# Performance work log

Measured on AMD Instinct MI355X. Metric: run time of the kernel, lower is better.

Reference implementation:

```python
import jax, jax.numpy as jnp
import numpy as np

D_MODEL, NHEAD, D_K = 512, 8, 64
MIN_RBF, MAX_RBF = 0.1, 0.9
MIN_SPREAD, MAX_SPREAD, BASE = 1.0, 6.0, 20.0
LN_EPS = 1e-5


def _layernorm(x, w, b):
    mu = jnp.mean(x, axis=-1, keepdims=True)
    var = jnp.var(x, axis=-1, keepdims=True)
    return (x - mu) * jax.lax.rsqrt(var + LN_EPS) * w + b


def setup_inputs() -> dict:
    key = jax.random.key(0)
    ks = jax.random.split(key, 10)
    B, N = 1, 2048
    inp = {
        "q": jax.random.normal(ks[0], (B, N, D_MODEL), jnp.float32),
        "k": jax.random.normal(ks[1], (B, N, D_MODEL), jnp.float32),
        "v": jax.random.normal(ks[2], (B, N, D_MODEL), jnp.float32),
        "coords": jax.random.normal(ks[3], (B, N, 3), jnp.float32) * 3.0,
        "key_padding_mask": jnp.zeros((B, N), bool),
        # learned params (torch.randn init for projections, LN defaults)
        "q_proj": jax.random.normal(ks[4], (NHEAD, D_MODEL, D_K), jnp.float32),
        "k_proj": jax.random.normal(ks[5], (NHEAD, D_MODEL, D_K), jnp.float32),
        "v_proj": jax.random.normal(ks[6], (NHEAD, D_MODEL, D_K), jnp.float32),
        "q_ln_w": jnp.ones((D_K,), jnp.float32), "q_ln_b": jnp.zeros((D_K,), jnp.float32),
        "k_ln_w": jnp.ones((D_K,), jnp.float32), "k_ln_b": jnp.zeros((D_K,), jnp.float32),
        "v_ln_w": jnp.ones((D_K,), jnp.float32), "v_ln_b": jnp.zeros((D_K,), jnp.float32),
        "out_w": jax.random.normal(ks[7], (D_MODEL, D_MODEL), jnp.float32) / np.sqrt(D_MODEL),
        "out_b": jnp.zeros((D_MODEL,), jnp.float32),
    }
    return inp


def reference(q, k, v, coords, key_padding_mask,
              q_proj, k_proj, v_proj,
              q_ln_w, q_ln_b, k_ln_w, k_ln_b, v_ln_w, v_ln_b,
              out_w, out_b):
    B, N, _ = q.shape
    # per-head projections: [B,H,N,dk]
    Q = _layernorm(jnp.einsum('bnd,hdk->bhnk', q, q_proj), q_ln_w, q_ln_b)
    K = _layernorm(jnp.einsum('bnd,hdk->bhnk', k, k_proj), k_ln_w, k_ln_b)
    V = _layernorm(jnp.einsum('bnd,hdk->bhnk', v, v_proj), v_ln_w, v_ln_b)

    # head-specific gaussian spreads (torch.logspace(0,1,H,base) semantics)
    spreads = MIN_SPREAD + (MAX_SPREAD - MIN_SPREAD) * (BASE ** jnp.linspace(0.0, 1.0, NHEAD) - 1.0) / (BASE - 1.0)

    # pairwise squared distances [B,N,N] -> per-head RBF [B,H,N,N]
    d2 = jnp.sum((coords[:, :, None, :] - coords[:, None, :, :]) ** 2, axis=-1)
    rbf = jnp.exp(-d2[:, None, :, :] / (2.0 * spreads[None, :, None, None] ** 2))
    rbf = jnp.clip(rbf, MIN_RBF, MAX_RBF)

    # RBF-modulated scaled dot-product attention
    scores = jnp.einsum('bhik,bhjk->bhij', Q, K) / np.sqrt(D_K) * rbf
    scores = jnp.where(key_padding_mask[:, None, None, :], -1e9, scores)
    P = jax.nn.softmax(scores, axis=-1)
    out = jnp.einsum('bhij,bhjk->bhik', P, V)  # [B,H,N,dk]

    # torch: out.permute(0,2,3,1).reshape(B,N,d_model)
    out = jnp.transpose(out, (0, 2, 3, 1)).reshape(B, N, D_MODEL)
    return out @ out_w.T + out_b
```

## Files before the change

kernel.cpp:

```cpp
#include <hip/hip_runtime.h>
#include <math.h>

#define N_TOK 2048
#define D_MODEL 512
#define NHEAD 8
#define DK 64
#define LOG2E 1.44269504f
#define QSCALE 0.18033688f
#define KTILE 6144
#define KHEAD (32 * KTILE)

typedef __attribute__((ext_vector_type(8))) short short8;
typedef __attribute__((ext_vector_type(4))) short short4v;
typedef __attribute__((ext_vector_type(4))) float f32x4;

__device__ __forceinline__ short f2bf(float x) {
    unsigned u = __float_as_uint(x);
    u = (u + 0x7fffu + ((u >> 16) & 1u)) >> 16;
    return (short)u;
}

__device__ __forceinline__ float bf2f(short s) {
    return __uint_as_float(((unsigned)(unsigned short)s) << 16);
}

__device__ __forceinline__ void split2(float x, short& h_, short& l_) {
    h_ = f2bf(x);
    l_ = f2bf(x - bf2f(h_));
}

__device__ __forceinline__ void split3(float x, short& h_, short& m_, short& l_) {
    h_ = f2bf(x);
    float r = x - bf2f(h_);
    m_ = f2bf(r);
    l_ = f2bf(r - bf2f(m_));
}

__device__ __forceinline__ unsigned cvt_pk_bf16(float lo, float hi) {
    unsigned r;
    asm("v_cvt_pk_bf16_f32 %0, %1, %2" : "=v"(r) : "v"(lo), "v"(hi));
    return r;
}

__device__ __forceinline__ float head_c(int h) {
    float tt = (float)h * (1.0f / 7.0f);
    float sp = 1.0f + 5.0f * (__builtin_exp2f(tt * 4.3219281f) - 1.0f) * (1.0f / 19.0f);
    return -LOG2E / (2.0f * sp * sp);
}

__global__ __launch_bounds__(256) void prep_all_kernel(
    const float* __restrict__ coords, const unsigned char* __restrict__ mask,
    const float* __restrict__ qp, const float* __restrict__ kp,
    const float* __restrict__ vp, const float* __restrict__ ow,
    short* __restrict__ Wt, short* __restrict__ Wo,
    short* __restrict__ Kf, float* __restrict__ mpen,
    unsigned* __restrict__ tflag)
{
    __shared__ float tile[64][65];
    const int bid = blockIdx.x;
    const int t = threadIdx.x;

    if (bid < 256) {
        int i = bid;
        int z = i >> 6;
        int bx = i & 7, by = (i >> 3) & 7;
        if (z == 3) {
            int m0 = bx * 64, j0 = by * 64, hh = by;
            for (int ii = t; ii < 4096; ii += 256) {
                int r = ii >> 6, kk = ii & 63;
                Wo[(size_t)(m0 + r) * 512 + j0 + kk] =
                    f2bf(ow[(size_t)(m0 + r) * 512 + kk * 8 + hh]);
            }
            return;
        }
        const float* src = z == 0 ? qp : (z == 1 ? kp : vp);
        const int h = bx, d0 = by * 64;
        for (int ii = t; ii < 4096; ii += 256) {
            int r = ii >> 6, c = ii & 63;
            tile[r][c] = src[((size_t)h * 512 + d0 + r) * 64 + c];
        }
        __syncthreads();
        short* W = Wt + (size_t)z * 512 * 512;
        for (int ii = t; ii < 4096; ii += 256) {
            int cr = ii >> 6, dc_ = ii & 63;
            W[(size_t)(h * 64 + cr) * 512 + d0 + dc_] = f2bf(tile[dc_][cr]);
        }
    } else {
        int j = (bid - 256) * 256 + t;
        float x = coords[j * 3 + 0], y = coords[j * 3 + 1], z = coords[j * 3 + 2];
        unsigned char mk = mask[j];
        mpen[j] = mk ? -1e9f : 0.f;
        unsigned long long b = __ballot(mk != 0);
        if ((t & 63) == 0) tflag[j >> 6] = (b != 0ull) ? 1u : 0u;
        float n2 = x * x + y * y + z * z;
        const short one = (short)0x3F80;
        const int kr = j & 15;
        #pragma unroll
        for (int h = 0; h < NHEAD; ++h) {
            float c = head_c(h);
            short ahx, alx, ahy, aly, ahz, alz, k2a, k2b, k2c;
            split2(-2.f * c * x, ahx, alx);
            split2(-2.f * c * y, ahy, aly);
            split2(-2.f * c * z, ahz, alz);
            split3(c * n2, k2a, k2b, k2c);
            short8 g0, g1, g2;
            g0[0] = ahx; g0[1] = alx; g0[2] = ahx; g0[3] = ahy;
            g0[4] = aly; g0[5] = ahy; g0[6] = ahz; g0[7] = alz;
            g1[0] = ahz; g1[1] = alx; g1[2] = aly; g1[3] = alz;
            g1[4] = k2a; g1[5] = k2b; g1[6] = k2c; g1[7] = one;
            g2[0] = one; g2[1] = one;
            #pragma unroll
            for (int e = 2; e < 8; ++e) g2[e] = 0;
            short8 g3;
            #pragma unroll
            for (int e = 0; e < 8; ++e) g3[e] = 0;
            short* base = Kf + (size_t)h * KHEAD + (size_t)(j >> 6) * KTILE
                        + 4096 + (size_t)((j >> 4) & 3) * 512;
            *(short8*)(base + (size_t)(0 * 16 + kr) * 8) = g0;
            *(short8*)(base + (size_t)(1 * 16 + kr) * 8) = g1;
            *(short8*)(base + (size_t)(2 * 16 + kr) * 8) = g2;
            *(short8*)(base + (size_t)(3 * 16 + kr) * 8) = g3;
        }
    }
}

__global__ __launch_bounds__(256) void proj_ln_mfma_kernel(
    const float* __restrict__ xq, const float* __restrict__ xk,
    const float* __restrict__ xv, const short* __restrict__ Wt,
    const float* __restrict__ qlw, const float* __restrict__ qlb,
    const float* __restrict__ klw, const float* __restrict__ klb,
    const float* __restrict__ vlw, const float* __restrict__ vlb,
    short* __restrict__ Qbf, short* __restrict__ Kf, short* __restrict__ Vf)
{
    __shared__ short Xs[128 * 64];
    __shared__ short Ws[64 * 64];
    const int z = blockIdx.z, h = blockIdx.y;
    const int n0 = blockIdx.x * 128;
    const int tid = threadIdx.x, w = tid >> 6, l = tid & 63;
    const int l15 = l & 15, lg = l >> 4;

    const float* X = z == 0 ? xq : (z == 1 ? xk : xv);
    const short* Wz = Wt + ((size_t)z * 512 + h * 64) * 512;

    const f32x4 zero4 = {0.f, 0.f, 0.f, 0.f};
    f32x4 acc[2][4];
    #pragma unroll
    for (int H = 0; H < 2; ++H)
        #pragma unroll
        for (int dc = 0; dc < 4; ++dc) acc[H][dc] = zero4;

    for (int kb = 0; kb < 8; ++kb) {
        const int d0 = kb * 64;
        __syncthreads();
        #pragma unroll
        for (int i = 0; i < 8; ++i) {
            int idx = tid + i * 256;
            int r = idx >> 4;
            int f = idx & 15;
            float4 xv4 = *(const float4*)(X + (size_t)(n0 + r) * 512 + d0 + f * 4);
            short4v pk;
            pk[0] = f2bf(xv4.x); pk[1] = f2bf(xv4.y);
            pk[2] = f2bf(xv4.z); pk[3] = f2bf(xv4.w);
            *(short4v*)(Xs + r * 64 + (((f >> 1) * 8) ^ ((r & 7) << 3)) + (f & 1) * 4) = pk;
        }
        #pragma unroll
        for (int i = 0; i < 2; ++i) {
            int c = tid + i * 256;
            int r = c >> 3, g = c & 7;
            short8 wv = *(const short8*)(Wz + (size_t)r * 512 + d0 + g * 8);
            *(short8*)(Ws + r * 64 + ((g * 8) ^ ((r & 7) << 3))) = wv;
        }
        __syncthreads();
        const int arowA = w * 16 + l15;
        const int arowB = 64 + arowA;
        const int asw = (arowA & 7) << 3;
        short8 aA0 = *(const short8*)(Xs + arowA * 64 + ((lg * 8) ^ asw));
        short8 aA1 = *(const short8*)(Xs + arowA * 64 + ((32 + lg * 8) ^ asw));
        short8 aB0 = *(const short8*)(Xs + arowB * 64 + ((lg * 8) ^ asw));
        short8 aB1 = *(const short8*)(Xs + arowB * 64 + ((32 + lg * 8) ^ asw));
        #pragma unroll
        for (int dc = 0; dc < 4; ++dc) {
            const int brow = dc * 16 + l15;
            short8 b0 = *(const short8*)(Ws + brow * 64 + ((lg * 8) ^ ((brow & 7) << 3)));
            short8 b1 = *(const short8*)(Ws + brow * 64 + ((32 + lg * 8) ^ ((brow & 7) << 3)));
            acc[0][dc] = __builtin_amdgcn_mfma_f32_16x16x32_bf16(aA0, b0, acc[0][dc], 0, 0, 0);
            acc[0][dc] = __builtin_amdgcn_mfma_f32_16x16x32_bf16(aA1, b1, acc[0][dc], 0, 0, 0);
            acc[1][dc] = __builtin_amdgcn_mfma_f32_16x16x32_bf16(aB0, b0, acc[1][dc], 0, 0, 0);
            acc[1][dc] = __builtin_amdgcn_mfma_f32_16x16x32_bf16(aB1, b1, acc[1][dc], 0, 0, 0);
        }
    }

    const float* lw  = z == 0 ? qlw : (z == 1 ? klw : vlw);
    const float* lbp = z == 0 ? qlb : (z == 1 ? klb : vlb);
    float wv_[4], bv_[4];
    #pragma unroll
    for (int dc = 0; dc < 4; ++dc) {
        wv_[dc] = lw[dc * 16 + l15];
        bv_[dc] = lbp[dc * 16 + l15];
    }

    #pragma unroll
    for (int H = 0; H < 2; ++H) {
        const int nb = n0 + H * 64;
        const int tile = nb >> 6;
        float mu[4], rs[4];
        #pragma unroll
        for (int reg = 0; reg < 4; ++reg) {
            float s = acc[H][0][reg] + acc[H][1][reg] + acc[H][2][reg] + acc[H][3][reg];
            #pragma unroll
            for (int off = 1; off < 16; off <<= 1) s += __shfl_xor(s, off);
            float m = s * (1.0f / 64.0f);
            float ss = 0.f;
            #pragma unroll
            for (int dc = 0; dc < 4; ++dc) { float d = acc[H][dc][reg] - m; ss += d * d; }
            #pragma unroll
            for (int off = 1; off < 16; off <<= 1) ss += __shfl_xor(ss, off);
            mu[reg] = m;
            rs[reg] = rsqrtf(ss * (1.0f / 64.0f) + 1e-5f);
        }
        if (z == 0) {
            #pragma unroll
            for (int dc = 0; dc < 4; ++dc)
                #pragma unroll
                for (int reg = 0; reg < 4; ++reg) {
                    int n = nb + w * 16 + lg * 4 + reg;
                    float val = ((acc[H][dc][reg] - mu[reg]) * rs[reg] * wv_[dc] + bv_[dc]) * QSCALE;
                    Qbf[((size_t)h * N_TOK + n) * DK + dc * 16 + l15] = f2bf(val);
                }
        } else if (z == 1) {
            short* Kh = Kf + (size_t)h * KHEAD;
            #pragma unroll
            for (int dc = 0; dc < 4; ++dc) {
                int hf  = dc >> 1;
                int lgc = ((dc & 1) << 1) | (l15 >> 3);
                int e   = l15 & 7;
                size_t base = (size_t)tile * KTILE + (w * 2 + hf) * 512 + 16 * 8 * lgc + e;
                #pragma unroll
                for (int reg = 0; reg < 4; ++reg) {
                    float val = (acc[H][dc][reg] - mu[reg]) * rs[reg] * wv_[dc] + bv_[dc];
                    Kh[base + (lg * 4 + reg) * 8] = f2bf(val);
                }
            }
        } else {
            short* Vh = Vf + (size_t)h * N_TOK * DK;
            int hfv = w >> 1;
            int lgv = ((w & 1) << 1) | (lg >> 1);
            int eb  = (lg & 1) * 4;
            #pragma unroll
            for (int dc = 0; dc < 4; ++dc) {
                short4v p;
                #pragma unroll
                for (int reg = 0; reg < 4; ++reg)
                    p[reg] = f2bf((acc[H][dc][reg] - mu[reg]) * rs[reg] * wv_[dc] + bv_[dc]);
                size_t addr = (size_t)tile * 4096 + (dc * 2 + hfv) * 512 + (l15 + 16 * lgv) * 8 + eb;
                *(short4v*)(Vh + addr) = p;
            }
        }
    }
}

__global__ __launch_bounds__(256) void attn_kernel(
    const short* __restrict__ Qbf, const short* __restrict__ Kf,
    const short* __restrict__ Vf, const float* __restrict__ coords,
    const float* __restrict__ mpen, const unsigned* __restrict__ tflag,
    short* __restrict__ PO, float* __restrict__ PL)
{
    __shared__ short Pls[4][1024];
    __shared__ float bufO[2][64][17];
    __shared__ float bufL[2][64];

    const int tid = threadIdx.x;
    const int w = tid >> 6, l = tid & 63;
    const int l15 = l & 15, lg = l >> 4;
    const int bid = blockIdx.x;
    const int h  = bid & 7;
    const int nt = (bid >> 3) & 127;
    const int z  = bid >> 10;
    const int n0 = nt * 16;

    char* Pb = (char*)&Pls[w][0];
    const int psw = (l15 & 7) << 4;

    const short* Qrow = Qbf + ((size_t)h * N_TOK + n0 + l15) * DK + lg * 8;
    const short8 qf0 = *(const short8*)(Qrow);
    const short8 qf1 = *(const short8*)(Qrow + 32);

    const float ch = head_c(h);
    const float qx = coords[(n0 + l15) * 3 + 0];
    const float qy = coords[(n0 + l15) * 3 + 1];
    const float qz = coords[(n0 + l15) * 3 + 2];
    const float cq2 = ch * (qx * qx + qy * qy + qz * qz);
    short8 qaug;
    {
        const short one = (short)0x3F80;
        short qhx, qlx, qhy, qly, qhz, qlz, q2a, q2b, q2c;
        split2(qx, qhx, qlx);
        split2(qy, qhy, qly);
        split2(qz, qhz, qlz);
        split3(cq2, q2a, q2b, q2c);
        #pragma unroll
        for (int e = 0; e < 8; ++e) qaug[e] = 0;
        if (lg == 0) {
            qaug[0] = qhx; qaug[1] = qhx; qaug[2] = qlx; qaug[3] = qhy;
            qaug[4] = qhy; qaug[5] = qly; qaug[6] = qhz; qaug[7] = qhz;
        } else if (lg == 1) {
            qaug[0] = qlz; qaug[1] = qlx; qaug[2] = qly; qaug[3] = qlz;
            qaug[4] = one; qaug[5] = one; qaug[6] = one; qaug[7] = q2a;
        } else if (lg == 2) {
            qaug[0] = q2b; qaug[1] = q2c;
        }
    }

    short8 ones8;
    #pragma unroll
    for (int i = 0; i < 8; ++i) ones8[i] = (short)0x3F80;

    const f32x4 zero4 = {0.f, 0.f, 0.f, 0.f};
    f32x4 oacc[4];
    f32x4 oacc_l = zero4;
    #pragma unroll
    for (int i = 0; i < 4; ++i) oacc[i] = zero4;

    const short* Kfh = Kf + (size_t)h * KHEAD;
    const short* Vfh = Vf + (size_t)h * N_TOK * DK;

    for (int t = 0; t < 4; ++t) {
        const int kt = (z * 4 + w) * 4 + t;
        const int kbase = kt * 64;
        const short* kp = Kfh + (size_t)kt * KTILE + l * 8;
        const short* ap = kp + 4096;
        const short* vp = Vfh + (size_t)kt * 4096 + l * 8;

        f32x4 sacc[4], aacc[4];
        #pragma unroll
        for (int nc = 0; nc < 4; ++nc) {
            short8 k0 = *(const short8*)(kp + nc * 1024);
            short8 k1 = *(const short8*)(kp + nc * 1024 + 512);
            short8 ka = *(const short8*)(ap + nc * 512);
            sacc[nc] = __builtin_amdgcn_mfma_f32_16x16x32_bf16(k0, qf0, zero4, 0, 0, 0);
            sacc[nc] = __builtin_amdgcn_mfma_f32_16x16x32_bf16(k1, qf1, sacc[nc], 0, 0, 0);
            aacc[nc] = __builtin_amdgcn_mfma_f32_16x16x32_bf16(ka, qaug, zero4, 0, 0, 0);
        }

        #pragma unroll
        for (int nc = 0; nc < 4; ++nc) {
            #pragma unroll
            for (int reg = 0; reg < 4; ++reg) {
                float rb = __builtin_exp2f(aacc[nc][reg]);
                rb = fminf(fmaxf(rb, 0.1f), 0.9f);
                sacc[nc][reg] *= rb;
            }
        }
        if (tflag[kt]) {
            #pragma unroll
            for (int nc = 0; nc < 4; ++nc)
                #pragma unroll
                for (int reg = 0; reg < 4; ++reg)
                    sacc[nc][reg] += mpen[kbase + nc * 16 + lg * 4 + reg];
        }

        #pragma unroll
        for (int nc = 0; nc < 4; ++nc) {
            float p0 = __builtin_exp2f(sacc[nc][0]);
            float p1 = __builtin_exp2f(sacc[nc][1]);
            float p2 = __builtin_exp2f(sacc[nc][2]);
            float p3 = __builtin_exp2f(sacc[nc][3]);
            uint2 u;
            u.x = cvt_pk_bf16(p0, p1);
            u.y = cvt_pk_bf16(p2, p3);
            *(uint2*)(Pb + ((l15 * 128 + nc * 32 + lg * 8) ^ psw)) = u;
        }

        short8 pf0 = *(const short8*)(Pb + ((l15 * 128 + lg * 16) ^ psw));
        short8 pf1 = *(const short8*)(Pb + ((l15 * 128 + 64 + lg * 16) ^ psw));
        #pragma unroll
        for (int dcc = 0; dcc < 4; ++dcc) {
            short8 v0 = *(const short8*)(vp + dcc * 1024);
            short8 v1 = *(const short8*)(vp + dcc * 1024 + 512);
            oacc[dcc] = __builtin_amdgcn_mfma_f32_16x16x32_bf16(v0, pf0, oacc[dcc], 0, 0, 0);
            oacc[dcc] = __builtin_amdgcn_mfma_f32_16x16x32_bf16(v1, pf1, oacc[dcc], 0, 0, 0);
        }
        oacc_l = __builtin_amdgcn_mfma_f32_16x16x32_bf16(ones8, pf0, oacc_l, 0, 0, 0);
        oacc_l = __builtin_amdgcn_mfma_f32_16x16x32_bf16(ones8, pf1, oacc_l, 0, 0, 0);
    }

    float l_ = oacc_l[0];

    if (w >= 2) {
        int slot = w - 2;
        bufL[slot][l] = l_;
        #pragma unroll
        for (int dc = 0; dc < 4; ++dc)
            #pragma unroll
            for (int reg = 0; reg < 4; ++reg)
                bufO[slot][l][dc * 4 + reg] = oacc[dc][reg];
    }
    __syncthreads();
    if (w < 2) {
        l_ += bufL[w][l];
        #pragma unroll
        for (int dc = 0; dc < 4; ++dc)
            #pragma unroll
            for (int reg = 0; reg < 4; ++reg)
                oacc[dc][reg] += bufO[w][l][dc * 4 + reg];
    }
    __syncthreads();
    if (w == 1) {
        bufL[0][l] = l_;
        #pragma unroll
        for (int dc = 0; dc < 4; ++dc)
            #pragma unroll
            for (int reg = 0; reg < 4; ++reg)
                bufO[0][l][dc * 4 + reg] = oacc[dc][reg];
    }
    __syncthreads();
    if (w == 0) {
        float lf = l_ + bufL[0][l];
        size_t p = ((size_t)z * NHEAD + h) * N_TOK + n0 + l15;
        if (lg == 0) PL[p] = lf;
        #pragma unroll
        for (int dcc = 0; dcc < 4; ++dcc) {
            short4v o4;
            #pragma unroll
            for (int reg = 0; reg < 4; ++reg)
                o4[reg] = f2bf(oacc[dcc][reg] + bufO[0][l][dcc * 4 + reg]);
            *(short4v*)(PO + p * 64 + dcc * 16 + lg * 4) = o4;
        }
    }
}

__global__ __launch_bounds__(256) void out_proj_kernel(
    const short* __restrict__ PO, const float* __restrict__ PL,
    const short* __restrict__ Wo, const float* __restrict__ bias,
    float* __restrict__ out)
{
    __shared__ short As[64 * 64];
    __shared__ short Bs[64 * 64];
    const int n0 = blockIdx.x * 64, m0 = blockIdx.y * 64;
    const int tid = threadIdx.x, w = tid >> 6, l = tid & 63;
    const int l15 = l & 15, lg = l >> 4;

    const f32x4 zero4 = {0.f, 0.f, 0.f, 0.f};
    f32x4 acc[4];
    #pragma unroll
    for (int dc = 0; dc < 4; ++dc) acc[dc] = zero4;

    for (int kb = 0; kb < 8; ++kb) {
        const int j0 = kb * 64;
        __syncthreads();
        #pragma unroll
        for (int i = 0; i < 2; ++i) {
            int c = tid + i * 256;
            int r = c >> 3, g = c & 7;
            int n = n0 + r;
            size_t p0 = (size_t)kb * N_TOK + n;
            size_t p1 = (size_t)(NHEAD + kb) * N_TOK + n;
            float rl = 1.0f / (PL[p0] + PL[p1]);
            short8 a0 = *(const short8*)(PO + p0 * 64 + g * 8);
            short8 a1 = *(const short8*)(PO + p1 * 64 + g * 8);
            short8 av;
            #pragma unroll
            for (int e = 0; e < 8; ++e)
                av[e] = f2bf((bf2f(a0[e]) + bf2f(a1[e])) * rl);
            *(short8*)(As + r * 64 + ((g * 8) ^ ((r & 7) << 3))) = av;
            short8 bv = *(const short8*)(Wo + (size_t)(m0 + r) * 512 + j0 + g * 8);
            *(short8*)(Bs + r * 64 + ((g * 8) ^ ((r & 7) << 3))) = bv;
        }
        __syncthreads();
        const int arow = w * 16 + l15;
        short8 a0 = *(const short8*)(As + arow * 64 + ((lg * 8) ^ ((arow & 7) << 3)));
        short8 a1 = *(const short8*)(As + arow * 64 + ((32 + lg * 8) ^ ((arow & 7) << 3)));
        #pragma unroll
        for (int dc = 0; dc < 4; ++dc) {
            const int brow = dc * 16 + l15;
            short8 b0 = *(const short8*)(Bs + brow * 64 + ((lg * 8) ^ ((brow & 7) << 3)));
            acc[dc] = __builtin_amdgcn_mfma_f32_16x16x32_bf16(a0, b0, acc[dc], 0, 0, 0);
            short8 b1 = *(const short8*)(Bs + brow * 64 + ((32 + lg * 8) ^ ((brow & 7) << 3)));
            acc[dc] = __builtin_amdgcn_mfma_f32_16x16x32_bf16(a1, b1, acc[dc], 0, 0, 0);
        }
    }

    #pragma unroll
    for (int dc = 0; dc < 4; ++dc) {
        float bm = bias[m0 + dc * 16 + l15];
        #pragma unroll
        for (int reg = 0; reg < 4; ++reg) {
            int n = n0 + w * 16 + lg * 4 + reg;
            out[(size_t)n * D_MODEL + m0 + dc * 16 + l15] = acc[dc][reg] + bm;
        }
    }
}

extern "C" void kernel_launch(void* const* d_in, const int* in_sizes, int n_in,
                              void* d_out, int out_size, void* d_ws, size_t ws_size,
                              hipStream_t stream)
{
    const float* q      = (const float*)d_in[0];
    const float* k      = (const float*)d_in[1];
    const float* v      = (const float*)d_in[2];
    const float* coords = (const float*)d_in[3];
    const unsigned char* mask = (const unsigned char*)d_in[4];
    const float* q_proj = (const float*)d_in[5];
    const float* k_proj = (const float*)d_in[6];
    const float* v_proj = (const float*)d_in[7];
    const float* q_ln_w = (const float*)d_in[8];
    const float* q_ln_b = (const float*)d_in[9];
    const float* k_ln_w = (const float*)d_in[10];
    const float* k_ln_b = (const float*)d_in[11];
    const float* v_ln_w = (const float*)d_in[12];
    const float* v_ln_b = (const float*)d_in[13];
    const float* out_w  = (const float*)d_in[14];
    const float* out_b  = (const float*)d_in[15];
    float* out = (float*)d_out;

    short* PO  = (short*)d_ws;
    short* Wt  = PO + 2097152;
    short* Wo  = Wt + 786432;
    short* Qbf = Wo + 262144;
    short* Kf  = Qbf + 1048576;
    short* Vf  = Kf + 1572864;
    float* mpen = (float*)(Vf + 1048576);
    unsigned* tflag = (unsigned*)(mpen + 2048);
    float* PL = (float*)(tflag + 32);

    prep_all_kernel<<<dim3(264), dim3(256), 0, stream>>>(
        coords, mask, q_proj, k_proj, v_proj, out_w, Wt, Wo, Kf, mpen, tflag);
    proj_ln_mfma_kernel<<<dim3(16, 8, 3), dim3(256), 0, stream>>>(
        q, k, v, Wt, q_ln_w, q_ln_b, k_ln_w, k_ln_b, v_ln_w, v_ln_b, Qbf, Kf, Vf);
    attn_kernel<<<dim3(2048), dim3(256), 0, stream>>>(
        Qbf, Kf, Vf, coords, mpen, tflag, PO, PL);
    out_proj_kernel<<<dim3(32, 8), dim3(256), 0, stream>>>(PO, PL, Wo, out_b, out);
}
```

Measured before the change: 67.88 us.

## Give each attention wave its own query rows, split keys four ways across blocks

Attention blocks now give each of their four waves a different 16-row query tile, with each block covering one quarter of the keys (eight 64-key tiles per wave). Before, the four waves of a block shared one query tile and split its keys. This removes the LDS reduction and the three block barriers at the end of the attention kernel and halves the grid. The cost is four partial outputs per head instead of two: PO workspace doubles, and the output projection must read and sum four partials per row, adding global traffic and extra bf16 rounding of the partial sums.

```diff
diff --git a/kernel.cpp b/kernel.cpp
--- a/kernel.cpp
+++ b/kernel.cpp
@@ -266,17 +266,16 @@
     short* __restrict__ PO, float* __restrict__ PL)
 {
     __shared__ short Pls[4][1024];
-    __shared__ float bufO[2][64][17];
-    __shared__ float bufL[2][64];
 
     const int tid = threadIdx.x;
     const int w = tid >> 6, l = tid & 63;
     const int l15 = l & 15, lg = l >> 4;
     const int bid = blockIdx.x;
     const int h  = bid & 7;
-    const int nt = (bid >> 3) & 127;
-    const int z  = bid >> 10;
-    const int n0 = nt * 16;
+    const int r2 = bid >> 3;
+    const int g  = r2 & 31;
+    const int z  = r2 >> 5;
+    const int n0 = g * 64 + w * 16;
 
     char* Pb = (char*)&Pls[w][0];
     const int psw = (l15 & 7) << 4;
@@ -324,8 +323,8 @@
     const short* Kfh = Kf + (size_t)h * KHEAD;
     const short* Vfh = Vf + (size_t)h * N_TOK * DK;
 
-    for (int t = 0; t < 4; ++t) {
-        const int kt = (z * 4 + w) * 4 + t;
+    for (int t = 0; t < 8; ++t) {
+        const int kt = z * 8 + t;
         const int kbase = kt * 64;
         const short* kp = Kfh + (size_t)kt * KTILE + l * 8;
         const short* ap = kp + 4096;
@@ -385,47 +384,15 @@
     }
 
     float l_ = oacc_l[0];
-
-    if (w >= 2) {
-        int slot = w - 2;
-        bufL[slot][l] = l_;
-        #pragma unroll
-        for (int dc = 0; dc < 4; ++dc)
-            #pragma unroll
-            for (int reg = 0; reg < 4; ++reg)
-                bufO[slot][l][dc * 4 + reg] = oacc[dc][reg];
-    }
-    __syncthreads();
-    if (w < 2) {
-        l_ += bufL[w][l];
-        #pragma unroll
-        for (int dc = 0; dc < 4; ++dc)
-            #pragma unroll
-            for (int reg = 0; reg < 4; ++reg)
-                oacc[dc][reg] += bufO[w][l][dc * 4 + reg];
-    }
-    __syncthreads();
-    if (w == 1) {
-        bufL[0][l] = l_;
-        #pragma unroll
-        for (int dc = 0; dc < 4; ++dc)
-            #pragma unroll
-            for (int reg = 0; reg < 4; ++reg)
-                bufO[0][l][dc * 4 + reg] = oacc[dc][reg];
-    }
-    __syncthreads();
-    if (w == 0) {
-        float lf = l_ + bufL[0][l];
-        size_t p = ((size_t)z * NHEAD + h) * N_TOK + n0 + l15;
-        if (lg == 0) PL[p] = lf;
-        #pragma unroll
-        for (int dcc = 0; dcc < 4; ++dcc) {
-            short4v o4;
-            #pragma unroll
-            for (int reg = 0; reg < 4; ++reg)
-                o4[reg] = f2bf(oacc[dcc][reg] + bufO[0][l][dcc * 4 + reg]);
-            *(short4v*)(PO + p * 64 + dcc * 16 + lg * 4) = o4;
-        }
+    size_t p = ((size_t)z * NHEAD + h) * N_TOK + n0 + l15;
+    if (lg == 0) PL[p] = l_;
+    #pragma unroll
+    for (int dcc = 0; dcc < 4; ++dcc) {
+        short4v o4;
+        #pragma unroll
+        for (int reg = 0; reg < 4; ++reg)
+            o4[reg] = f2bf(oacc[dcc][reg]);
+        *(short4v*)(PO + p * 64 + dcc * 16 + lg * 4) = o4;
     }
 }
 
@@ -455,13 +422,18 @@
             int n = n0 + r;
             size_t p0 = (size_t)kb * N_TOK + n;
             size_t p1 = (size_t)(NHEAD + kb) * N_TOK + n;
-            float rl = 1.0f / (PL[p0] + PL[p1]);
+            size_t p2 = (size_t)(2 * NHEAD + kb) * N_TOK + n;
+            size_t p3 = (size_t)(3 * NHEAD + kb) * N_TOK + n;
+            float rl = 1.0f / (PL[p0] + PL[p1] + PL[p2] + PL[p3]);
             short8 a0 = *(const short8*)(PO + p0 * 64 + g * 8);
             short8 a1 = *(const short8*)(PO + p1 * 64 + g * 8);
+            short8 a2 = *(const short8*)(PO + p2 * 64 + g * 8);
+            short8 a3 = *(const short8*)(PO + p3 * 64 + g * 8);
             short8 av;
             #pragma unroll
             for (int e = 0; e < 8; ++e)
-                av[e] = f2bf((bf2f(a0[e]) + bf2f(a1[e])) * rl);
+                av[e] = f2bf(((bf2f(a0[e]) + bf2f(a1[e])) +
+                              (bf2f(a2[e]) + bf2f(a3[e]))) * rl);
             *(short8*)(As + r * 64 + ((g * 8) ^ ((r & 7) << 3))) = av;
             short8 bv = *(const short8*)(Wo + (size_t)(m0 + r) * 512 + j0 + g * 8);
             *(short8*)(Bs + r * 64 + ((g * 8) ^ ((r & 7) << 3))) = bv;
@@ -514,7 +486,7 @@
     float* out = (float*)d_out;
 
     short* PO  = (short*)d_ws;
-    short* Wt  = PO + 2097152;
+    short* Wt  = PO + 4194304;
     short* Wo  = Wt + 786432;
     short* Qbf = Wo + 262144;
     short* Kf  = Qbf + 1048576;
@@ -527,7 +499,7 @@
         coords, mask, q_proj, k_proj, v_proj, out_w, Wt, Wo, Kf, mpen, tflag);
     proj_ln_mfma_kernel<<<dim3(16, 8, 3), dim3(256), 0, stream>>>(
         q, k, v, Wt, q_ln_w, q_ln_b, k_ln_w, k_ln_b, v_ln_w, v_ln_b, Qbf, Kf, Vf);
-    attn_kernel<<<dim3(2048), dim3(256), 0, stream>>>(
+    attn_kernel<<<dim3(1024), dim3(256), 0, stream>>>(
         Qbf, Kf, Vf, coords, mpen, tflag, PO, PL);
     out_proj_kernel<<<dim3(32, 8), dim3(256), 0, stream>>>(PO, PL, Wo, out_b, out);
 }
```

New measurement: 71.21 us. 4.9% more time.

## Switch attention to 32x32x16 MFMA with 32-query tiles and register P exchange

Applied to the files above, without the earlier changes.

Attention now uses 32x32x16 bf16 MFMA instructions over 32-query tiles instead of 16x16x32 over 16-query tiles, which halves the number of attention blocks. The producer kernels write Q, K, V and the RBF augmentation into new fragment layouts that match the larger MFMA. The P matrix is passed between lanes with cross-half shuffles instead of a swizzled LDS round trip. The row sum is now taken with scalar adds rather than a ones-MFMA. The larger tiles give more K/V reuse per load and fewer LDS operations, at the cost of more registers per wave and scalar bf16 stores in the output epilogue.

```diff
diff --git a/kernel.cpp b/kernel.cpp
--- a/kernel.cpp
+++ b/kernel.cpp
@@ -13,6 +13,8 @@
 typedef __attribute__((ext_vector_type(8))) short short8;
 typedef __attribute__((ext_vector_type(4))) short short4v;
 typedef __attribute__((ext_vector_type(4))) float f32x4;
+typedef __attribute__((ext_vector_type(16))) float f32x16;
+typedef __attribute__((ext_vector_type(4))) unsigned int u32x4;
 
 __device__ __forceinline__ short f2bf(float x) {
     unsigned u = __float_as_uint(x);
@@ -94,7 +96,8 @@
         if ((t & 63) == 0) tflag[j >> 6] = (b != 0ull) ? 1u : 0u;
         float n2 = x * x + y * y + z * z;
         const short one = (short)0x3F80;
-        const int kr = j & 15;
+        const int s = (j & 63) >> 5;
+        const int m = j & 31;
         #pragma unroll
         for (int h = 0; h < NHEAD; ++h) {
             float c = head_c(h);
@@ -103,7 +106,7 @@
             split2(-2.f * c * y, ahy, aly);
             split2(-2.f * c * z, ahz, alz);
             split3(c * n2, k2a, k2b, k2c);
-            short8 g0, g1, g2;
+            short8 g0, g1, g2, g3;
             g0[0] = ahx; g0[1] = alx; g0[2] = ahx; g0[3] = ahy;
             g0[4] = aly; g0[5] = ahy; g0[6] = ahz; g0[7] = alz;
             g1[0] = ahz; g1[1] = alx; g1[2] = aly; g1[3] = alz;
@@ -111,15 +114,14 @@
             g2[0] = one; g2[1] = one;
             #pragma unroll
             for (int e = 2; e < 8; ++e) g2[e] = 0;
-            short8 g3;
             #pragma unroll
             for (int e = 0; e < 8; ++e) g3[e] = 0;
             short* base = Kf + (size_t)h * KHEAD + (size_t)(j >> 6) * KTILE
-                        + 4096 + (size_t)((j >> 4) & 3) * 512;
-            *(short8*)(base + (size_t)(0 * 16 + kr) * 8) = g0;
-            *(short8*)(base + (size_t)(1 * 16 + kr) * 8) = g1;
-            *(short8*)(base + (size_t)(2 * 16 + kr) * 8) = g2;
-            *(short8*)(base + (size_t)(3 * 16 + kr) * 8) = g3;
+                        + 4096 + (size_t)s * 1024;
+            *(short8*)(base + (size_t)m * 8) = g0;
+            *(short8*)(base + (size_t)(m + 32) * 8) = g1;
+            *(short8*)(base + 512 + (size_t)m * 8) = g2;
+            *(short8*)(base + 512 + (size_t)(m + 32) * 8) = g3;
         }
     }
 }
@@ -130,7 +132,7 @@
     const float* __restrict__ qlw, const float* __restrict__ qlb,
     const float* __restrict__ klw, const float* __restrict__ klb,
     const float* __restrict__ vlw, const float* __restrict__ vlb,
-    short* __restrict__ Qbf, short* __restrict__ Kf, short* __restrict__ Vf)
+    short* __restrict__ Qf, short* __restrict__ Kf, short* __restrict__ Vf)
 {
     __shared__ short Xs[128 * 64];
     __shared__ short Ws[64 * 64];
@@ -202,7 +204,7 @@
     #pragma unroll
     for (int H = 0; H < 2; ++H) {
         const int nb = n0 + H * 64;
-        const int tile = nb >> 6;
+        const int kt = nb >> 6;
         float mu[4], rs[4];
         #pragma unroll
         for (int reg = 0; reg < 4; ++reg) {
@@ -219,40 +221,45 @@
             rs[reg] = rsqrtf(ss * (1.0f / 64.0f) + 1e-5f);
         }
         if (z == 0) {
+            short* Qh = Qf + (size_t)h * (N_TOK * DK);
             #pragma unroll
             for (int dc = 0; dc < 4; ++dc)
                 #pragma unroll
                 for (int reg = 0; reg < 4; ++reg) {
                     int n = nb + w * 16 + lg * 4 + reg;
                     float val = ((acc[H][dc][reg] - mu[reg]) * rs[reg] * wv_[dc] + bv_[dc]) * QSCALE;
-                    Qbf[((size_t)h * N_TOK + n) * DK + dc * 16 + l15] = f2bf(val);
+                    size_t addr = (size_t)(n >> 5) * 2048 + dc * 512
+                                + ((n & 31) + 32 * (l15 >> 3)) * 8 + (l15 & 7);
+                    Qh[addr] = f2bf(val);
                 }
         } else if (z == 1) {
             short* Kh = Kf + (size_t)h * KHEAD;
-            #pragma unroll
-            for (int dc = 0; dc < 4; ++dc) {
-                int hf  = dc >> 1;
-                int lgc = ((dc & 1) << 1) | (l15 >> 3);
-                int e   = l15 & 7;
-                size_t base = (size_t)tile * KTILE + (w * 2 + hf) * 512 + 16 * 8 * lgc + e;
+            const int sA = w >> 1;
+            const int mA = (w & 1) * 16 + lg * 4;
+            #pragma unroll
+            for (int dc = 0; dc < 4; ++dc)
                 #pragma unroll
                 for (int reg = 0; reg < 4; ++reg) {
                     float val = (acc[H][dc][reg] - mu[reg]) * rs[reg] * wv_[dc] + bv_[dc];
-                    Kh[base + (lg * 4 + reg) * 8] = f2bf(val);
+                    size_t addr = (size_t)kt * KTILE + sA * 2048 + dc * 512
+                                + (mA + reg + 32 * (l15 >> 3)) * 8 + (l15 & 7);
+                    Kh[addr] = f2bf(val);
                 }
-            }
         } else {
-            short* Vh = Vf + (size_t)h * N_TOK * DK;
-            int hfv = w >> 1;
-            int lgv = ((w & 1) << 1) | (lg >> 1);
-            int eb  = (lg & 1) * 4;
+            short* Vh = Vf + (size_t)h * (N_TOK * DK);
+            const int kc = w;
+            const int g = lg >> 1;
+            const int e0 = (lg & 1) * 4;
             #pragma unroll
             for (int dc = 0; dc < 4; ++dc) {
+                int dt = dc >> 1;
+                int m = (dc & 1) * 16 + l15;
                 short4v p;
                 #pragma unroll
                 for (int reg = 0; reg < 4; ++reg)
                     p[reg] = f2bf((acc[H][dc][reg] - mu[reg]) * rs[reg] * wv_[dc] + bv_[dc]);
-                size_t addr = (size_t)tile * 4096 + (dc * 2 + hfv) * 512 + (l15 + 16 * lgv) * 8 + eb;
+                size_t addr = (size_t)kt * 4096 + dt * 2048 + kc * 512
+                            + (m + 32 * g) * 8 + e0;
                 *(short4v*)(Vh + addr) = p;
             }
         }
@@ -260,37 +267,37 @@
 }
 
 __global__ __launch_bounds__(256) void attn_kernel(
-    const short* __restrict__ Qbf, const short* __restrict__ Kf,
+    const short* __restrict__ Qf, const short* __restrict__ Kf,
     const short* __restrict__ Vf, const float* __restrict__ coords,
     const float* __restrict__ mpen, const unsigned* __restrict__ tflag,
     short* __restrict__ PO, float* __restrict__ PL)
 {
-    __shared__ short Pls[4][1024];
-    __shared__ float bufO[2][64][17];
-    __shared__ float bufL[2][64];
+    __shared__ float bufO[2][32][65];
+    __shared__ float bufL[2][32];
 
     const int tid = threadIdx.x;
     const int w = tid >> 6, l = tid & 63;
-    const int l15 = l & 15, lg = l >> 4;
+    const int q31 = l & 31;
+    const bool hi = (l >= 32);
+    const int rbase = hi ? 4 : 0;
     const int bid = blockIdx.x;
     const int h  = bid & 7;
-    const int nt = (bid >> 3) & 127;
-    const int z  = bid >> 10;
-    const int n0 = nt * 16;
-
-    char* Pb = (char*)&Pls[w][0];
-    const int psw = (l15 & 7) << 4;
-
-    const short* Qrow = Qbf + ((size_t)h * N_TOK + n0 + l15) * DK + lg * 8;
-    const short8 qf0 = *(const short8*)(Qrow);
-    const short8 qf1 = *(const short8*)(Qrow + 32);
+    const int qt = (bid >> 3) & 63;
+    const int z  = bid >> 9;
+    const int n0 = qt * 32;
+
+    const short* qbase = Qf + (size_t)h * (N_TOK * DK) + (size_t)qt * 2048 + l * 8;
+    short8 qf[4];
+    #pragma unroll
+    for (int c = 0; c < 4; ++c) qf[c] = *(const short8*)(qbase + c * 512);
 
     const float ch = head_c(h);
-    const float qx = coords[(n0 + l15) * 3 + 0];
-    const float qy = coords[(n0 + l15) * 3 + 1];
-    const float qz = coords[(n0 + l15) * 3 + 2];
+    const int qn = n0 + q31;
+    const float qx = coords[qn * 3 + 0];
+    const float qy = coords[qn * 3 + 1];
+    const float qz = coords[qn * 3 + 2];
     const float cq2 = ch * (qx * qx + qy * qy + qz * qz);
-    short8 qaug;
+    short8 qaug0, qaug1;
     {
         const short one = (short)0x3F80;
         short qhx, qlx, qhy, qly, qhz, qlz, q2a, q2b, q2c;
@@ -298,133 +305,151 @@
         split2(qy, qhy, qly);
         split2(qz, qhz, qlz);
         split3(cq2, q2a, q2b, q2c);
-        #pragma unroll
-        for (int e = 0; e < 8; ++e) qaug[e] = 0;
-        if (lg == 0) {
-            qaug[0] = qhx; qaug[1] = qhx; qaug[2] = qlx; qaug[3] = qhy;
-            qaug[4] = qhy; qaug[5] = qly; qaug[6] = qhz; qaug[7] = qhz;
-        } else if (lg == 1) {
-            qaug[0] = qlz; qaug[1] = qlx; qaug[2] = qly; qaug[3] = qlz;
-            qaug[4] = one; qaug[5] = one; qaug[6] = one; qaug[7] = q2a;
-        } else if (lg == 2) {
-            qaug[0] = q2b; qaug[1] = q2c;
-        }
-    }
-
-    short8 ones8;
-    #pragma unroll
-    for (int i = 0; i < 8; ++i) ones8[i] = (short)0x3F80;
-
-    const f32x4 zero4 = {0.f, 0.f, 0.f, 0.f};
-    f32x4 oacc[4];
-    f32x4 oacc_l = zero4;
-    #pragma unroll
-    for (int i = 0; i < 4; ++i) oacc[i] = zero4;
+        if (!hi) {
+            qaug0[0] = qhx; qaug0[1] = qhx; qaug0[2] = qlx; qaug0[3] = qhy;
+            qaug0[4] = qhy; qaug0[5] = qly; qaug0[6] = qhz; qaug0[7] = qhz;
+            qaug1[0] = q2b; qaug1[1] = q2c;
+            #pragma unroll
+            for (int e = 2; e < 8; ++e) qaug1[e] = 0;
+        } else {
+            qaug0[0] = qlz; qaug0[1] = qlx; qaug0[2] = qly; qaug0[3] = qlz;
+            qaug0[4] = one; qaug0[5] = one; qaug0[6] = one; qaug0[7] = q2a;
+            #pragma unroll
+            for (int e = 0; e < 8; ++e) qaug1[e] = 0;
+        }
+    }
+
+    const f32x16 zero16 = {0,0,0,0, 0,0,0,0, 0,0,0,0, 0,0,0,0};
+    f32x16 oacc0 = zero16, oacc1 = zero16;
+    float l_ = 0.f;
 
     const short* Kfh = Kf + (size_t)h * KHEAD;
-    const short* Vfh = Vf + (size_t)h * N_TOK * DK;
+    const short* Vfh = Vf + (size_t)h * (N_TOK * DK);
 
     for (int t = 0; t < 4; ++t) {
-        const int kt = (z * 4 + w) * 4 + t;
+        const int kt = z * 16 + w * 4 + t;
         const int kbase = kt * 64;
-        const short* kp = Kfh + (size_t)kt * KTILE + l * 8;
-        const short* ap = kp + 4096;
-        const short* vp = Vfh + (size_t)kt * 4096 + l * 8;
-
-        f32x4 sacc[4], aacc[4];
-        #pragma unroll
-        for (int nc = 0; nc < 4; ++nc) {
-            short8 k0 = *(const short8*)(kp + nc * 1024);
-            short8 k1 = *(const short8*)(kp + nc * 1024 + 512);
-            short8 ka = *(const short8*)(ap + nc * 512);
-            sacc[nc] = __builtin_amdgcn_mfma_f32_16x16x32_bf16(k0, qf0, zero4, 0, 0, 0);
-            sacc[nc] = __builtin_amdgcn_mfma_f32_16x16x32_bf16(k1, qf1, sacc[nc], 0, 0, 0);
-            aacc[nc] = __builtin_amdgcn_mfma_f32_16x16x32_bf16(ka, qaug, zero4, 0, 0, 0);
-        }
-
-        #pragma unroll
-        for (int nc = 0; nc < 4; ++nc) {
-            #pragma unroll
-            for (int reg = 0; reg < 4; ++reg) {
-                float rb = __builtin_exp2f(aacc[nc][reg]);
+        #pragma unroll
+        for (int s = 0; s < 2; ++s) {
+            const short* kp = Kfh + (size_t)kt * KTILE + s * 2048 + l * 8;
+            const short* ap = Kfh + (size_t)kt * KTILE + 4096 + s * 1024 + l * 8;
+            const short* vp = Vfh + (size_t)kt * 4096 + s * 1024 + l * 8;
+
+            f32x16 sacc = zero16, aacc = zero16;
+            #pragma unroll
+            for (int c = 0; c < 4; ++c) {
+                short8 kfr = *(const short8*)(kp + c * 512);
+                sacc = __builtin_amdgcn_mfma_f32_32x32x16_bf16(kfr, qf[c], sacc, 0, 0, 0);
+            }
+            {
+                short8 a0 = *(const short8*)(ap);
+                short8 a1 = *(const short8*)(ap + 512);
+                aacc = __builtin_amdgcn_mfma_f32_32x32x16_bf16(a0, qaug0, aacc, 0, 0, 0);
+                aacc = __builtin_amdgcn_mfma_f32_32x32x16_bf16(a1, qaug1, aacc, 0, 0, 0);
+            }
+
+            #pragma unroll
+            for (int r = 0; r < 16; ++r) {
+                float rb = __builtin_exp2f(aacc[r]);
                 rb = fminf(fmaxf(rb, 0.1f), 0.9f);
-                sacc[nc][reg] *= rb;
-            }
-        }
-        if (tflag[kt]) {
-            #pragma unroll
-            for (int nc = 0; nc < 4; ++nc)
+                sacc[r] *= rb;
+            }
+            if (tflag[kt]) {
                 #pragma unroll
-                for (int reg = 0; reg < 4; ++reg)
-                    sacc[nc][reg] += mpen[kbase + nc * 16 + lg * 4 + reg];
-        }
-
-        #pragma unroll
-        for (int nc = 0; nc < 4; ++nc) {
-            float p0 = __builtin_exp2f(sacc[nc][0]);
-            float p1 = __builtin_exp2f(sacc[nc][1]);
-            float p2 = __builtin_exp2f(sacc[nc][2]);
-            float p3 = __builtin_exp2f(sacc[nc][3]);
-            uint2 u;
-            u.x = cvt_pk_bf16(p0, p1);
-            u.y = cvt_pk_bf16(p2, p3);
-            *(uint2*)(Pb + ((l15 * 128 + nc * 32 + lg * 8) ^ psw)) = u;
-        }
-
-        short8 pf0 = *(const short8*)(Pb + ((l15 * 128 + lg * 16) ^ psw));
-        short8 pf1 = *(const short8*)(Pb + ((l15 * 128 + 64 + lg * 16) ^ psw));
-        #pragma unroll
-        for (int dcc = 0; dcc < 4; ++dcc) {
-            short8 v0 = *(const short8*)(vp + dcc * 1024);
-            short8 v1 = *(const short8*)(vp + dcc * 1024 + 512);
-            oacc[dcc] = __builtin_amdgcn_mfma_f32_16x16x32_bf16(v0, pf0, oacc[dcc], 0, 0, 0);
-            oacc[dcc] = __builtin_amdgcn_mfma_f32_16x16x32_bf16(v1, pf1, oacc[dcc], 0, 0, 0);
-        }
-        oacc_l = __builtin_amdgcn_mfma_f32_16x16x32_bf16(ones8, pf0, oacc_l, 0, 0, 0);
-        oacc_l = __builtin_amdgcn_mfma_f32_16x16x32_bf16(ones8, pf1, oacc_l, 0, 0, 0);
-    }
-
-    float l_ = oacc_l[0];
+                for (int r = 0; r < 16; ++r)
+                    sacc[r] += mpen[kbase + s * 32 + ((r & 3) + 8 * (r >> 2) + rbase)];
+            }
+
+            #pragma unroll
+            for (int r = 0; r < 16; ++r) sacc[r] = __builtin_exp2f(sacc[r]);
+            {
+                float s01 = (sacc[0] + sacc[1]) + (sacc[2] + sacc[3]);
+                float s23 = (sacc[4] + sacc[5]) + (sacc[6] + sacc[7]);
+                float s45 = (sacc[8] + sacc[9]) + (sacc[10] + sacc[11]);
+                float s67 = (sacc[12] + sacc[13]) + (sacc[14] + sacc[15]);
+                l_ += (s01 + s23) + (s45 + s67);
+            }
+
+            unsigned U0 = cvt_pk_bf16(sacc[0], sacc[1]);
+            unsigned U1 = cvt_pk_bf16(sacc[2], sacc[3]);
+            unsigned U2 = cvt_pk_bf16(sacc[4], sacc[5]);
+            unsigned U3 = cvt_pk_bf16(sacc[6], sacc[7]);
+            unsigned U4 = cvt_pk_bf16(sacc[8], sacc[9]);
+            unsigned U5 = cvt_pk_bf16(sacc[10], sacc[11]);
+            unsigned U6 = cvt_pk_bf16(sacc[12], sacc[13]);
+            unsigned U7 = cvt_pk_bf16(sacc[14], sacc[15]);
+            unsigned W0 = (unsigned)__shfl_xor((int)U0, 32);
+            unsigned W1 = (unsigned)__shfl_xor((int)U1, 32);
+            unsigned W2 = (unsigned)__shfl_xor((int)U2, 32);
+            unsigned W3 = (unsigned)__shfl_xor((int)U3, 32);
+            unsigned W4 = (unsigned)__shfl_xor((int)U4, 32);
+            unsigned W5 = (unsigned)__shfl_xor((int)U5, 32);
+            unsigned W6 = (unsigned)__shfl_xor((int)U6, 32);
+            unsigned W7 = (unsigned)__shfl_xor((int)U7, 32);
+
+            u32x4 b0v, b1v;
+            b0v[0] = hi ? W2 : U0;  b0v[1] = hi ? W3 : U1;
+            b0v[2] = hi ? U2 : W0;  b0v[3] = hi ? U3 : W1;
+            b1v[0] = hi ? W6 : U4;  b1v[1] = hi ? W7 : U5;
+            b1v[2] = hi ? U6 : W4;  b1v[3] = hi ? U7 : W5;
+            short8 pb0 = __builtin_bit_cast(short8, b0v);
+            short8 pb1 = __builtin_bit_cast(short8, b1v);
+
+            {
+                short8 v00 = *(const short8*)(vp);
+                short8 v01 = *(const short8*)(vp + 512);
+                short8 v10 = *(const short8*)(vp + 2048);
+                short8 v11 = *(const short8*)(vp + 2048 + 512);
+                oacc0 = __builtin_amdgcn_mfma_f32_32x32x16_bf16(v00, pb0, oacc0, 0, 0, 0);
+                oacc0 = __builtin_amdgcn_mfma_f32_32x32x16_bf16(v01, pb1, oacc0, 0, 0, 0);
+                oacc1 = __builtin_amdgcn_mfma_f32_32x32x16_bf16(v10, pb0, oacc1, 0, 0, 0);
+                oacc1 = __builtin_amdgcn_mfma_f32_32x32x16_bf16(v11, pb1, oacc1, 0, 0, 0);
+            }
+        }
+    }
+
+    l_ += __shfl_xor(l_, 32);
 
     if (w >= 2) {
         int slot = w - 2;
-        bufL[slot][l] = l_;
-        #pragma unroll
-        for (int dc = 0; dc < 4; ++dc)
-            #pragma unroll
-            for (int reg = 0; reg < 4; ++reg)
-                bufO[slot][l][dc * 4 + reg] = oacc[dc][reg];
+        if (!hi) bufL[slot][q31] = l_;
+        #pragma unroll
+        for (int r = 0; r < 16; ++r) {
+            int d = (r & 3) + 8 * (r >> 2) + rbase;
+            bufO[slot][q31][d] = oacc0[r];
+            bufO[slot][q31][32 + d] = oacc1[r];
+        }
     }
     __syncthreads();
     if (w < 2) {
-        l_ += bufL[w][l];
-        #pragma unroll
-        for (int dc = 0; dc < 4; ++dc)
-            #pragma unroll
-            for (int reg = 0; reg < 4; ++reg)
-                oacc[dc][reg] += bufO[w][l][dc * 4 + reg];
+        l_ += bufL[w][q31];
+        #pragma unroll
+        for (int r = 0; r < 16; ++r) {
+            int d = (r & 3) + 8 * (r >> 2) + rbase;
+            oacc0[r] += bufO[w][q31][d];
+            oacc1[r] += bufO[w][q31][32 + d];
+        }
     }
     __syncthreads();
     if (w == 1) {
-        bufL[0][l] = l_;
-        #pragma unroll
-        for (int dc = 0; dc < 4; ++dc)
-            #pragma unroll
-            for (int reg = 0; reg < 4; ++reg)
-                bufO[0][l][dc * 4 + reg] = oacc[dc][reg];
+        if (!hi) bufL[0][q31] = l_;
+        #pragma unroll
+        for (int r = 0; r < 16; ++r) {
+            int d = (r & 3) + 8 * (r >> 2) + rbase;
+            bufO[0][q31][d] = oacc0[r];
+            bufO[0][q31][32 + d] = oacc1[r];
+        }
     }
     __syncthreads();
     if (w == 0) {
-        float lf = l_ + bufL[0][l];
-        size_t p = ((size_t)z * NHEAD + h) * N_TOK + n0 + l15;
-        if (lg == 0) PL[p] = lf;
-        #pragma unroll
-        for (int dcc = 0; dcc < 4; ++dcc) {
-            short4v o4;
-            #pragma unroll
-            for (int reg = 0; reg < 4; ++reg)
-                o4[reg] = f2bf(oacc[dcc][reg] + bufO[0][l][dcc * 4 + reg]);
-            *(short4v*)(PO + p * 64 + dcc * 16 + lg * 4) = o4;
+        l_ += bufL[0][q31];
+        size_t p = ((size_t)z * NHEAD + h) * N_TOK + n0 + q31;
+        if (!hi) PL[p] = l_;
+        #pragma unroll
+        for (int r = 0; r < 16; ++r) {
+            int d = (r & 3) + 8 * (r >> 2) + rbase;
+            PO[p * 64 + d] = f2bf(oacc0[r] + bufO[0][q31][d]);
+            PO[p * 64 + 32 + d] = f2bf(oacc1[r] + bufO[0][q31][32 + d]);
         }
     }
 }
@@ -516,8 +541,8 @@
     short* PO  = (short*)d_ws;
     short* Wt  = PO + 2097152;
     short* Wo  = Wt + 786432;
-    short* Qbf = Wo + 262144;
-    short* Kf  = Qbf + 1048576;
+    short* Qf  = Wo + 262144;
+    short* Kf  = Qf + 1048576;
     short* Vf  = Kf + 1572864;
     float* mpen = (float*)(Vf + 1048576);
     unsigned* tflag = (unsigned*)(mpen + 2048);
@@ -526,8 +551,8 @@
     prep_all_kernel<<<dim3(264), dim3(256), 0, stream>>>(
         coords, mask, q_proj, k_proj, v_proj, out_w, Wt, Wo, Kf, mpen, tflag);
     proj_ln_mfma_kernel<<<dim3(16, 8, 3), dim3(256), 0, stream>>>(
-        q, k, v, Wt, q_ln_w, q_ln_b, k_ln_w, k_ln_b, v_ln_w, v_ln_b, Qbf, Kf, Vf);
-    attn_kernel<<<dim3(2048), dim3(256), 0, stream>>>(
-        Qbf, Kf, Vf, coords, mpen, tflag, PO, PL);
+        q, k, v, Wt, q_ln_w, q_ln_b, k_ln_w, k_ln_b, v_ln_w, v_ln_b, Qf, Kf, Vf);
+    attn_kernel<<<dim3(1024), dim3(256), 0, stream>>>(
+        Qf, Kf, Vf, coords, mpen, tflag, PO, PL);
     out_proj_kernel<<<dim3(32, 8), dim3(256), 0, stream>>>(PO, PL, Wo, out_b, out);
 }
```

Measured after the change: 67.18 us. Within noise of the previous version (-1.0%).
